# Performance work log

Measured on AMD Instinct MI355X. Metric: run time of the kernel, lower is better.

The kernel has to match this reference:

```python
import jax, jax.numpy as jnp
import numpy as np

VEC = 90  # per-anchor vector length: obj(1)+box(4)+1 unused? -> layout: [p, dx, dy, dw, dh, _, 12 point, 72 seg]


def _decode(out, thresh, t, anchors, case):
    """Dense, mask-based version of Detector._filter + Detector._parse.

    The torch code gathers rows via nonzero (data-dependent shape); for a
    jit-compatible reference we decode every cell and zero out rows whose
    sigmoid(objectness) <= thresh. Row layout matches torch exactly:
    [n, sigmoid(p), cx, cy, w, h, point(12), seg(72)].
    """
    B, C, H, W = out.shape
    v = jnp.transpose(out, (0, 2, 3, 1)).reshape(B, H, W, 3, VEC)
    p = v[..., 0]
    mask = jax.nn.sigmoid(p) > thresh                      # [B,H,W,3]
    iy = jnp.arange(H, dtype=v.dtype)[None, :, None, None]
    ix = jnp.arange(W, dtype=v.dtype)[None, None, :, None]
    cy = (iy + v[..., 2]) * t
    cx = (ix + v[..., 1]) * t
    w = anchors[:, 0] * jnp.exp(v[..., 3])                 # broadcast over anchor dim
    h = anchors[:, 1] * jnp.exp(v[..., 4])
    s = jnp.sqrt(w * w + h * h) / case                     # diagonal / case, [B,H,W,3]
    point = v[..., 6:18] * s[..., None]                    # 6 (x,y) keypoint pairs scaled
    seg = v[..., 18:90].reshape(B, H, W, 3, 24, 3)         # 24 triplets (coord, sig, sig)
    seg = jnp.concatenate(
        [seg[..., :1] * s[..., None, None], jax.nn.sigmoid(seg[..., 1:3])],
        axis=-1).reshape(B, H, W, 3, 72)
    n = jnp.broadcast_to(jnp.arange(B, dtype=v.dtype)[:, None, None, None], p.shape)
    obj = jnp.stack([n, jax.nn.sigmoid(p), cx, cy, w, h], axis=-1)
    rows = jnp.concatenate([obj, point, seg], axis=-1).reshape(-1, VEC)
    return jnp.where(mask.reshape(-1, 1), rows, jnp.zeros((), rows.dtype))


def setup_inputs() -> dict:
    key = jax.random.key(0)
    ks = jax.random.split(key, 7)
    B = 32
    return {
        "out13": jax.random.normal(ks[0], (B, 270, 13, 13), jnp.float32),
        "out26": jax.random.normal(ks[1], (B, 270, 26, 26), jnp.float32),
        "out52": jax.random.normal(ks[2], (B, 270, 52, 52), jnp.float32),
        "anchors13": jax.random.uniform(ks[3], (3, 2), jnp.float32, 50.0, 300.0),
        "anchors26": jax.random.uniform(ks[4], (3, 2), jnp.float32, 20.0, 120.0),
        "anchors52": jax.random.uniform(ks[5], (3, 2), jnp.float32, 5.0, 60.0),
        "thresh": jax.random.uniform(ks[6], (1,), jnp.float32, 0.4, 0.7),
        "case": 416,
    }


def reference(out13, out26, out52, anchors13, anchors26, anchors52, thresh, case):
    th = thresh[0]
    c = jnp.float32(case)
    boxes = jnp.concatenate([
        _decode(out13, th, jnp.float32(32.0), anchors13, c),
        _decode(out26, th, jnp.float32(16.0), anchors26, c),
        _decode(out52, th, jnp.float32(8.0), anchors52, c),
    ], axis=0)
    return boxes
```

## Files before the change

kernel.cpp:

```cpp
#include <hip/hip_runtime.h>
#include <math.h>

#define PX 32
#define NT 192

__device__ __forceinline__ float sigf(float x) { return 1.0f / (1.0f + expf(-x)); }

template<int H, int W, int T, bool F4>
__device__ __forceinline__ void decode_level(
    const float* __restrict__ in, const float* __restrict__ anchors,
    float th, float invCase, float* __restrict__ out, long gRowBase,
    int blkL, float* __restrict__ lds)
{
    constexpr int HW = H * W;
    constexpr int SPANS = (HW + PX - 1) / PX;
    const int b    = blkL / SPANS;
    const int P0   = (blkL % SPANS) * PX;
    const int npix = (HW - P0 < PX) ? (HW - P0) : PX;

    const int a    = threadIdx.x >> 6;
    const int lane = threadIdx.x & 63;
    const int h    = lane >> 5;
    const int p    = lane & 31;

    if (p < npix) {
        const int pix = P0 + p;
        const int x   = pix % W;
        const int y   = pix / W;
        const float* src = in + ((long)b * 270 + a * 90 + 45 * h) * HW + pix;

        float v[45];
        #pragma unroll
        for (int j = 0; j < 45; ++j) v[j] = src[(long)j * HW];

        float sp = sigf(v[0]);
        bool  m  = sp > th;
        float A0 = anchors[a * 2 + 0], A1 = anchors[a * 2 + 1];
        float w  = A0 * expf(v[3]);
        float hb = A1 * expf(v[4]);
        float s  = sqrtf(w * w + hb * hb) * invCase;
        float cx = ((float)x + v[1]) * (float)T;
        float cy = ((float)y + v[2]) * (float)T;

        float ms = __shfl(m ? s : 0.0f, p, 64);
        float mf = __shfl(m ? 1.0f : 0.0f, p, 64);
        const bool mB = mf > 0.5f;

        float* dst = lds + (p * 3 + a) * 90 + 45 * h;
        #pragma unroll
        for (int j = 0; j < 45; ++j) {
            float val = v[j];
            bool coordAlways = (j % 3 == 0);
            bool pointRegion = (j >= 6 && j < 18);
            float rv;
            if (coordAlways)      rv = val * ms;
            else if (pointRegion) rv = (h == 0) ? val * ms : (mB ? sigf(val) : 0.0f);
            else                  rv = mB ? sigf(val) : 0.0f;
            dst[j] = rv;
        }
        if (h == 0) {
            dst[0] = m ? (float)b : 0.0f;
            dst[1] = m ? sp       : 0.0f;
            dst[2] = m ? cx       : 0.0f;
            dst[3] = m ? cy       : 0.0f;
            dst[4] = m ? w        : 0.0f;
            dst[5] = m ? hb       : 0.0f;
        }
    }
    __syncthreads();

    const int nfl = npix * 3 * 90;
    const size_t gbase = (size_t)(gRowBase + ((long)b * HW + P0) * 3) * 90;
    if (F4) {
        float4* d4 = (float4*)(out + gbase);
        const float4* s4 = (const float4*)lds;
        for (int i = threadIdx.x; i < (nfl >> 2); i += NT) d4[i] = s4[i];
    } else {
        float2* d2 = (float2*)(out + gbase);
        const float2* s2 = (const float2*)lds;
        for (int i = threadIdx.x; i < (nfl >> 1); i += NT) d2[i] = s2[i];
    }
}

__global__ __launch_bounds__(NT, 3) void decode_all(
    const float* __restrict__ in13, const float* __restrict__ in26,
    const float* __restrict__ in52,
    const float* __restrict__ anc13, const float* __restrict__ anc26,
    const float* __restrict__ anc52,
    const float* __restrict__ thresh, const int* __restrict__ casep,
    float* __restrict__ out, int nblk52, int nblk26, long rows13, long rows26)
{
    __shared__ float lds[PX * 3 * 90];
    const float th = thresh[0];
    const float invCase = 1.0f / (float)(*casep);
    const int blk = blockIdx.x;

    if (blk < nblk52)
        decode_level<52, 52, 8, true>(in52, anc52, th, invCase, out,
                                      rows13 + rows26, blk, lds);
    else if (blk < nblk52 + nblk26)
        decode_level<26, 26, 16, true>(in26, anc26, th, invCase, out,
                                       rows13, blk - nblk52, lds);
    else
        decode_level<13, 13, 32, false>(in13, anc13, th, invCase, out,
                                        0, blk - nblk52 - nblk26, lds);
}

extern "C" void kernel_launch(void* const* d_in, const int* in_sizes, int n_in,
                              void* d_out, int out_size, void* d_ws, size_t ws_size,
                              hipStream_t stream) {
    const float* in13  = (const float*)d_in[0];
    const float* in26  = (const float*)d_in[1];
    const float* in52  = (const float*)d_in[2];
    const float* anc13 = (const float*)d_in[3];
    const float* anc26 = (const float*)d_in[4];
    const float* anc52 = (const float*)d_in[5];
    const float* th    = (const float*)d_in[6];
    const int*   casep = (const int*)d_in[7];
    float* out = (float*)d_out;

    int B = in_sizes[0] / (270 * 13 * 13);

    long rows13 = (long)B * 13 * 13 * 3;
    long rows26 = (long)B * 26 * 26 * 3;

    int nblk13 = B * ((13 * 13 + PX - 1) / PX);
    int nblk26 = B * ((26 * 26 + PX - 1) / PX);
    int nblk52 = B * ((52 * 52 + PX - 1) / PX);

    decode_all<<<dim3(nblk52 + nblk26 + nblk13), dim3(NT), 0, stream>>>(
        in13, in26, in52, anc13, anc26, anc52, th, casep, out,
        nblk52, nblk26, rows13, rows26);
}
```

Before: 56.63 us.

## Halve LDS staging buffer with two-pass flush to raise occupancy

The LDS staging buffer shrinks to half the pixels (16 instead of 32 per block). Results stay in registers and are written out in two passes, each with its own block-wide barrier and global flush. With roughly half the shared memory per block, launch bounds go from 3 to 6 blocks per SIMD/CU, aiming for more waves in flight to hide memory latency. In exchange it adds extra barriers and serialised flushes per block, and puts more register pressure on the 45 live values under the tighter launch bound.

```diff
diff --git a/kernel.cpp b/kernel.cpp
--- a/kernel.cpp
+++ b/kernel.cpp
@@ -3,8 +3,27 @@
 
 #define PX 32
 #define NT 192
+#define HPX 16
+#define LROWS (HPX * 3)
 
 __device__ __forceinline__ float sigf(float x) { return 1.0f / (1.0f + expf(-x)); }
+
+template<bool F4>
+__device__ __forceinline__ void flushLds(const float* __restrict__ lds,
+                                         float* __restrict__ outp, int nfl, int tid)
+{
+    if (F4) {
+        float4* d4 = (float4*)outp;
+        const float4* s4 = (const float4*)lds;
+        for (int i = tid; i < (nfl >> 2); i += NT) d4[i] = s4[i];
+        int rem = nfl & 3, tail = nfl & ~3;
+        if (tid < rem) outp[tail + tid] = lds[tail + tid];
+    } else {
+        float2* d2 = (float2*)outp;
+        const float2* s2 = (const float2*)lds;
+        for (int i = tid; i < (nfl >> 1); i += NT) d2[i] = s2[i];
+    }
+}
 
 template<int H, int W, int T, bool F4>
 __device__ __forceinline__ void decode_level(
@@ -18,18 +37,20 @@
     const int P0   = (blkL % SPANS) * PX;
     const int npix = (HW - P0 < PX) ? (HW - P0) : PX;
 
-    const int a    = threadIdx.x >> 6;
-    const int lane = threadIdx.x & 63;
+    const int tid  = threadIdx.x;
+    const int a    = tid >> 6;
+    const int lane = tid & 63;
     const int h    = lane >> 5;
     const int p    = lane & 31;
+    const bool act = (p < npix);
 
-    if (p < npix) {
+    float v[45];
+    if (act) {
         const int pix = P0 + p;
         const int x   = pix % W;
         const int y   = pix / W;
         const float* src = in + ((long)b * 270 + a * 90 + 45 * h) * HW + pix;
 
-        float v[45];
         #pragma unroll
         for (int j = 0; j < 45; ++j) v[j] = src[(long)j * HW];
 
@@ -46,43 +67,50 @@
         float mf = __shfl(m ? 1.0f : 0.0f, p, 64);
         const bool mB = mf > 0.5f;
 
-        float* dst = lds + (p * 3 + a) * 90 + 45 * h;
         #pragma unroll
         for (int j = 0; j < 45; ++j) {
             float val = v[j];
             bool coordAlways = (j % 3 == 0);
             bool pointRegion = (j >= 6 && j < 18);
-            float rv;
-            if (coordAlways)      rv = val * ms;
-            else if (pointRegion) rv = (h == 0) ? val * ms : (mB ? sigf(val) : 0.0f);
-            else                  rv = mB ? sigf(val) : 0.0f;
-            dst[j] = rv;
+            if (coordAlways)      v[j] = val * ms;
+            else if (pointRegion) v[j] = (h == 0) ? val * ms : (mB ? sigf(val) : 0.0f);
+            else                  v[j] = mB ? sigf(val) : 0.0f;
         }
         if (h == 0) {
-            dst[0] = m ? (float)b : 0.0f;
-            dst[1] = m ? sp       : 0.0f;
-            dst[2] = m ? cx       : 0.0f;
-            dst[3] = m ? cy       : 0.0f;
-            dst[4] = m ? w        : 0.0f;
-            dst[5] = m ? hb       : 0.0f;
+            v[0] = m ? (float)b : 0.0f;
+            v[1] = m ? sp       : 0.0f;
+            v[2] = m ? cx       : 0.0f;
+            v[3] = m ? cy       : 0.0f;
+            v[4] = m ? w        : 0.0f;
+            v[5] = m ? hb       : 0.0f;
         }
     }
+
+    const size_t gbase = (size_t)(gRowBase + ((long)b * HW + P0) * 3) * 90;
+
+    if (act && p < HPX) {
+        float* dst = lds + (p * 3 + a) * 90 + 45 * h;
+        #pragma unroll
+        for (int j = 0; j < 45; ++j) dst[j] = v[j];
+    }
     __syncthreads();
+    int npixA = npix < HPX ? npix : HPX;
+    flushLds<F4>(lds, out + gbase, npixA * 3 * 90, tid);
 
-    const int nfl = npix * 3 * 90;
-    const size_t gbase = (size_t)(gRowBase + ((long)b * HW + P0) * 3) * 90;
-    if (F4) {
-        float4* d4 = (float4*)(out + gbase);
-        const float4* s4 = (const float4*)lds;
-        for (int i = threadIdx.x; i < (nfl >> 2); i += NT) d4[i] = s4[i];
-    } else {
-        float2* d2 = (float2*)(out + gbase);
-        const float2* s2 = (const float2*)lds;
-        for (int i = threadIdx.x; i < (nfl >> 1); i += NT) d2[i] = s2[i];
+    int npixB = npix - HPX;
+    if (npixB > 0) {
+        __syncthreads();
+        if (act && p >= HPX) {
+            float* dst = lds + ((p - HPX) * 3 + a) * 90 + 45 * h;
+            #pragma unroll
+            for (int j = 0; j < 45; ++j) dst[j] = v[j];
+        }
+        __syncthreads();
+        flushLds<F4>(lds, out + gbase + (size_t)LROWS * 90, npixB * 3 * 90, tid);
     }
 }
 
-__global__ __launch_bounds__(NT, 3) void decode_all(
+__global__ __launch_bounds__(NT, 6) void decode_all(
     const float* __restrict__ in13, const float* __restrict__ in26,
     const float* __restrict__ in52,
     const float* __restrict__ anc13, const float* __restrict__ anc26,
@@ -90,7 +118,7 @@
     const float* __restrict__ thresh, const int* __restrict__ casep,
     float* __restrict__ out, int nblk52, int nblk26, long rows13, long rows26)
 {
-    __shared__ float lds[PX * 3 * 90];
+    __shared__ float lds[LROWS * 90];
     const float th = thresh[0];
     const float invCase = 1.0f / (float)(*casep);
     const int blk = blockIdx.x;
```

Result: faster. 54.52 us (-3.7%).
